# Performance work log

Measured on AMD Instinct MI355X. Metric: run time of the kernel, lower is better.

## Reference

```python
import jax, jax.numpy as jnp
import numpy as np

D = 2048          # hidden_size
N = 16            # num query heads
K = 8             # num kv heads
G = N // K        # GQA groups
H = 128           # head_dim (== head_dim_original, already padded)
T_NOISE = 1024
T_PAD = 1024
MAX_KV = 4096
THETA = 1000000.0
EPS = 1e-6
SM_SCALE = H ** -0.5
NEG = -1e30


def apply_rope(x, pos):
    # x: (T, heads, H); rotate-half (NeoX/Qwen) convention over full head_dim
    half = H // 2
    inv_freq = 1.0 / (THETA ** (jnp.arange(half, dtype=jnp.float32) / half))
    ang = pos.astype(jnp.float32)[:, None] * inv_freq[None, :]      # (T, half)
    cos = jnp.cos(ang)[:, None, :]
    sin = jnp.sin(ang)[:, None, :]
    x1, x2 = x[..., :half], x[..., half:]
    return jnp.concatenate([x1 * cos - x2 * sin, x2 * cos + x1 * sin], axis=-1)


def rms_norm(x, scale):
    var = jnp.mean(jnp.square(x), axis=-1, keepdims=True)
    return x * jax.lax.rsqrt(var + EPS) * scale


def setup_inputs() -> dict:
    key = jax.random.key(0)
    ks = jax.random.split(key, 10)
    cache_len = 1024
    actual_ctx = 768
    u = lambda k, shape: jax.random.uniform(k, shape, jnp.float32) * 0.01  # nnx uniform init
    return {
        "x_noise": jax.random.normal(ks[0], (T_NOISE, D), jnp.float32),
        "target_hidden": jax.random.normal(ks[1], (T_PAD, D), jnp.float32),
        "noise_positions": jnp.arange(T_NOISE, dtype=jnp.int32) + cache_len + actual_ctx,
        "ctx_positions": jnp.arange(T_PAD, dtype=jnp.int32) + cache_len,
        "kv_cache_k": jax.random.normal(ks[2], (1, N, MAX_KV, H), jnp.float32),
        "kv_cache_v": jax.random.normal(ks[3], (1, N, MAX_KV, H), jnp.float32),
        "cache_len": cache_len,
        "actual_ctx_count": actual_ctx,
        "Wq": u(ks[4], (D, N, H)),
        "Wk": u(ks[5], (D, K, H)),
        "Wv": u(ks[6], (D, K, H)),
        "Wo": u(ks[7], (N, H, D)),
        "q_scale": u(ks[8], (H,)),
        "k_scale": u(ks[9], (H,)),
    }


def reference(x_noise, target_hidden, noise_positions, ctx_positions,
              kv_cache_k, kv_cache_v, cache_len, actual_ctx_count,
              Wq, Wk, Wv, Wo, q_scale, k_scale):
    T_noise = x_noise.shape[0]
    T_padded = target_hidden.shape[0]
    # Q projection + RMSNorm + RoPE
    q = jnp.einsum('td,dnh->tnh', x_noise, Wq)
    q = apply_rope(rms_norm(q, q_scale), noise_positions)              # (Tq, N, H)
    # K/V over [context, noise]
    x_new = jnp.concatenate([target_hidden, x_noise], axis=0)
    k_new = jnp.einsum('td,dkh->tkh', x_new, Wk)
    v_new = jnp.einsum('td,dkh->tkh', x_new, Wv)
    new_positions = jnp.concatenate([ctx_positions, noise_positions], axis=0)
    k_new = apply_rope(rms_norm(k_new, k_scale), new_positions)
    # GQA expand before cache write (matches original)
    if G > 1:
        k_new = jnp.repeat(k_new, G, axis=1)
        v_new = jnp.repeat(v_new, G, axis=1)
    # Phase A: masked context write at cache_len
    ctx_mask = (jnp.arange(T_padded) < actual_ctx_count)[:, None, None]
    k_ctx = jnp.where(ctx_mask, k_new[:T_padded], 0.0)
    v_ctx = jnp.where(ctx_mask, v_new[:T_padded], 0.0)
    to4d = lambda a: a.transpose(1, 0, 2)[None]                        # (1, N, T, H)
    kv_cache_k = jax.lax.dynamic_update_slice(kv_cache_k, to4d(k_ctx), (0, 0, cache_len, 0))
    kv_cache_v = jax.lax.dynamic_update_slice(kv_cache_v, to4d(v_ctx), (0, 0, cache_len, 0))
    # Phase B: noise write at cache_len + actual_ctx_count
    noise_start = cache_len + actual_ctx_count
    kv_cache_k = jax.lax.dynamic_update_slice(kv_cache_k, to4d(k_new[T_padded:]), (0, 0, noise_start, 0))
    kv_cache_v = jax.lax.dynamic_update_slice(kv_cache_v, to4d(v_new[T_padded:]), (0, 0, noise_start, 0))
    new_cache_len = noise_start + T_noise
    # Non-causal attention over full cache, padding masked (segment_ids semantics)
    kv_valid = jnp.arange(MAX_KV) < new_cache_len                      # (MAX_KV,)
    scores = jnp.einsum('qnh,nkh->nqk', q, kv_cache_k[0]) * SM_SCALE   # (N, Tq, MAX_KV)
    scores = jnp.where(kv_valid[None, None, :], scores, NEG)
    probs = jax.nn.softmax(scores, axis=-1)
    attn = jnp.einsum('nqk,nkh->qnh', probs, kv_cache_v[0])            # (Tq, N, H)
    output = jnp.einsum('qnh,nhd->qd', attn, Wo)                       # (Tq, D)
    return (output, kv_cache_k, kv_cache_v)
```

## Files before the change

kernel.cpp:

```cpp
#include <hip/hip_runtime.h>
#include <hip/hip_bf16.h>
#include <math.h>

#define D 2048
#define NH 16
#define KHD 8
#define HD 128
#define T_NOISE 1024
#define T_PAD 1024
#define MAX_KV 4096
#define SM_SCALE 0.08838834764831845f

typedef __attribute__((ext_vector_type(8))) short short8;
typedef __attribute__((ext_vector_type(4))) short short4v;
typedef __attribute__((ext_vector_type(4))) float f32x4;

__device__ __forceinline__ unsigned short f2bf(float f) {
    union { float f; unsigned u; } v; v.f = f;
    unsigned r = v.u + 0x7fff + ((v.u >> 16) & 1);
    return (unsigned short)(r >> 16);
}
__device__ __forceinline__ float bf2f(short s) {
    union { unsigned u; float f; } v; v.u = ((unsigned)(unsigned short)s) << 16;
    return v.f;
}
__device__ __forceinline__ void gload16(const void* g, void* l) {
    __builtin_amdgcn_global_load_lds(
        (const __attribute__((address_space(1))) unsigned int*)g,
        (__attribute__((address_space(3))) unsigned int*)l, 16, 0, 0);
}
__device__ __forceinline__ unsigned cvtpk(float lo, float hi) {
    unsigned r;
    asm("v_cvt_pk_bf16_f32 %0, %1, %2" : "=v"(r) : "v"(lo), "v"(hi));
    return r;
}

__global__ __launch_bounds__(256)
void cast_concat(const float* __restrict__ A0, const float* __restrict__ A1,
                 short* __restrict__ out, int splitElems) {
    int i = (blockIdx.x * 256 + threadIdx.x) * 8;
    const float* src = (i < splitElems) ? (A0 + i) : (A1 + (i - splitElems));
    float4 f0 = *(const float4*)src;
    float4 f1 = *(const float4*)(src + 4);
    short8 s;
    s[0] = (short)f2bf(f0.x); s[1] = (short)f2bf(f0.y);
    s[2] = (short)f2bf(f0.z); s[3] = (short)f2bf(f0.w);
    s[4] = (short)f2bf(f1.x); s[5] = (short)f2bf(f1.y);
    s[6] = (short)f2bf(f1.z); s[7] = (short)f2bf(f1.w);
    *(short8*)(out + i) = s;
}

__global__ __launch_bounds__(256)
void conv_transpose(const float* __restrict__ W, short* __restrict__ Wt,
                    int R, int C) {
    __shared__ short t[64][72];
    int tid = threadIdx.x;
    int r0 = blockIdx.y * 64, c0 = blockIdx.x * 64;
    int rl = tid >> 4, cl4 = (tid & 15) * 4;
    #pragma unroll
    for (int j = 0; j < 4; ++j) {
        int r = rl + j * 16;
        float4 f = *(const float4*)(W + (size_t)(r0 + r) * C + c0 + cl4);
        t[cl4 + 0][r] = (short)f2bf(f.x);
        t[cl4 + 1][r] = (short)f2bf(f.y);
        t[cl4 + 2][r] = (short)f2bf(f.z);
        t[cl4 + 3][r] = (short)f2bf(f.w);
    }
    __syncthreads();
    #pragma unroll
    for (int j = 0; j < 2; ++j) {
        int idx = tid + j * 256;
        int cr = idx >> 3, rc8 = (idx & 7) * 8;
        *(short8*)(Wt + (size_t)(c0 + cr) * R + r0 + rc8) = *(const short8*)&t[cr][rc8];
    }
}

__global__ __launch_bounds__(256)
void gemm_qkv(const short* __restrict__ xbf, const short* __restrict__ Btp,
              short* __restrict__ k_tmpb, short* __restrict__ v_tmpb,
              short* __restrict__ q_tmpb) {
    const int n0 = blockIdx.x * 128;
    const int m0 = blockIdx.y * 128;
    const bool isQ = (n0 >= 2048);
    if (isQ && m0 >= 1024) return;
    const short* A = xbf + (isQ ? (size_t)1024 * 2048 : 0);

    __shared__ __align__(16) short As[128 * 32];
    __shared__ __align__(16) short Bs[128 * 32];
    const int tid = threadIdx.x;
    const int w = tid >> 6, lane = tid & 63;
    const int g = lane >> 4, li = lane & 15;
    const int wr = w >> 1, wc = w & 1;

    f32x4 acc[4][4];
    #pragma unroll
    for (int mi = 0; mi < 4; ++mi)
        #pragma unroll
        for (int ni = 0; ni < 4; ++ni) {
            acc[mi][ni][0] = 0.f; acc[mi][ni][1] = 0.f;
            acc[mi][ni][2] = 0.f; acc[mi][ni][3] = 0.f;
        }

    for (int k0 = 0; k0 < 2048; k0 += 32) {
        #pragma unroll
        for (int i = 0; i < 2; ++i) {
            int idx = i * 256 + w * 64 + lane;
            int row = idx >> 2, slot = idx & 3;
            gload16(A + (size_t)(m0 + row) * 2048 + k0 + slot * 8,
                    (char*)As + (size_t)(i * 256 + w * 64) * 16);
            gload16(Btp + (size_t)(n0 + row) * 2048 + k0 + slot * 8,
                    (char*)Bs + (size_t)(i * 256 + w * 64) * 16);
        }
        __syncthreads();
        short8 af[4], bf[4];
        #pragma unroll
        for (int mi = 0; mi < 4; ++mi)
            af[mi] = *(const short8*)&As[(wr * 64 + mi * 16 + li) * 32 + g * 8];
        #pragma unroll
        for (int ni = 0; ni < 4; ++ni)
            bf[ni] = *(const short8*)&Bs[(wc * 64 + ni * 16 + li) * 32 + g * 8];
        #pragma unroll
        for (int mi = 0; mi < 4; ++mi)
            #pragma unroll
            for (int ni = 0; ni < 4; ++ni)
                acc[mi][ni] = __builtin_amdgcn_mfma_f32_16x16x32_bf16(
                    af[mi], bf[ni], acc[mi][ni], 0, 0, 0);
        __syncthreads();
    }
    short* cp; int cbase, ldc2;
    if (n0 < 1024)      { cp = k_tmpb; cbase = 0;    ldc2 = 1024; }
    else if (n0 < 2048) { cp = v_tmpb; cbase = 1024; ldc2 = 1024; }
    else                { cp = q_tmpb; cbase = 2048; ldc2 = 2048; }
    #pragma unroll
    for (int mi = 0; mi < 4; ++mi)
        #pragma unroll
        for (int ni = 0; ni < 4; ++ni) {
            int n = n0 + wc * 64 + ni * 16 + li - cbase;
            #pragma unroll
            for (int r = 0; r < 4; ++r) {
                int m = m0 + wr * 64 + mi * 16 + 4 * g + r;
                cp[(size_t)m * ldc2 + n] = (short)f2bf(acc[mi][ni][r]);
            }
        }
}

__global__ __launch_bounds__(256)
void gemm_bf16_64(const short* __restrict__ A, const short* __restrict__ Bt,
                  float* __restrict__ C, int ldc, int K) {
    __shared__ __align__(16) short As[64 * 32];
    __shared__ __align__(16) short Bs[128 * 32];
    const int tid = threadIdx.x;
    const int w = tid >> 6, lane = tid & 63;
    const int g = lane >> 4, li = lane & 15;
    const int wr = w >> 1, wc = w & 1;
    const int m0 = blockIdx.y * 64, n0 = blockIdx.x * 128;

    f32x4 acc[2][4];
    #pragma unroll
    for (int mi = 0; mi < 2; ++mi)
        #pragma unroll
        for (int ni = 0; ni < 4; ++ni) {
            acc[mi][ni][0] = 0.f; acc[mi][ni][1] = 0.f;
            acc[mi][ni][2] = 0.f; acc[mi][ni][3] = 0.f;
        }

    for (int k0 = 0; k0 < K; k0 += 32) {
        {
            int idx = w * 64 + lane;
            int row = idx >> 2, slot = idx & 3;
            gload16(A + (size_t)(m0 + row) * K + k0 + slot * 8,
                    (char*)As + (size_t)(w * 64) * 16);
        }
        #pragma unroll
        for (int i = 0; i < 2; ++i) {
            int idx = i * 256 + w * 64 + lane;
            int row = idx >> 2, slot = idx & 3;
            gload16(Bt + (size_t)(n0 + row) * K + k0 + slot * 8,
                    (char*)Bs + (size_t)(i * 256 + w * 64) * 16);
        }
        __syncthreads();
        short8 af[2], bf[4];
        #pragma unroll
        for (int mi = 0; mi < 2; ++mi)
            af[mi] = *(const short8*)&As[(wr * 32 + mi * 16 + li) * 32 + g * 8];
        #pragma unroll
        for (int ni = 0; ni < 4; ++ni)
            bf[ni] = *(const short8*)&Bs[(wc * 64 + ni * 16 + li) * 32 + g * 8];
        #pragma unroll
        for (int mi = 0; mi < 2; ++mi)
            #pragma unroll
            for (int ni = 0; ni < 4; ++ni)
                acc[mi][ni] = __builtin_amdgcn_mfma_f32_16x16x32_bf16(
                    af[mi], bf[ni], acc[mi][ni], 0, 0, 0);
        __syncthreads();
    }
    #pragma unroll
    for (int mi = 0; mi < 2; ++mi)
        #pragma unroll
        for (int ni = 0; ni < 4; ++ni) {
            int n = n0 + wc * 64 + ni * 16 + li;
            #pragma unroll
            for (int r = 0; r < 4; ++r) {
                int m = m0 + wr * 32 + mi * 16 + 4 * g + r;
                C[(size_t)m * ldc + n] = acc[mi][ni][r];
            }
        }
}

__global__ __launch_bounds__(128)
void rmsrope_bf(short* __restrict__ x, int hpt,
                const int* __restrict__ posA, const int* __restrict__ posB,
                int splitT, const float* __restrict__ scale, float post) {
    __shared__ float red[128];
    __shared__ float nrm[128];
    int row = blockIdx.x;
    int h = threadIdx.x;
    float v = bf2f(x[(size_t)row * HD + h]);
    red[h] = v * v;
    __syncthreads();
    #pragma unroll
    for (int off = 64; off > 0; off >>= 1) {
        if (h < off) red[h] += red[h + off];
        __syncthreads();
    }
    float inv = rsqrtf(red[0] * (1.0f / 128.0f) + 1e-6f);
    nrm[h] = v * inv * scale[h];
    __syncthreads();
    if (h < 64) {
        int t = row / hpt;
        int pos = (t < splitT) ? posA[t] : posB[t - splitT];
        float inv_freq = expf((float)h * (-13.815510557964274f / 64.0f));
        float ang = (float)pos * inv_freq;
        float c = cosf(ang), s = sinf(ang);
        float x1 = nrm[h], x2 = nrm[h + 64];
        x[(size_t)row * HD + h]      = (short)f2bf((x1 * c - x2 * s) * post);
        x[(size_t)row * HD + h + 64] = (short)f2bf((x2 * c + x1 * s) * post);
    }
}

__global__ __launch_bounds__(256)
void cache_scatter2(const float* __restrict__ in_k, const float* __restrict__ in_v,
                    const short* __restrict__ k_tmpb, const short* __restrict__ v_tmpb,
                    float* __restrict__ out_k, float* __restrict__ out_v,
                    short* __restrict__ kbf, short* __restrict__ vbf,
                    const int* __restrict__ clp, const int* __restrict__ acp) {
    const int cache_len = clp[0], actx = acp[0];
    const int noise_start = cache_len + actx;
    const int new_len = noise_start + T_NOISE;
    int i = blockIdx.x * 256 + threadIdx.x;
    int n = i >> 16;
    int rem = i & 65535;
    int pos = rem >> 4;
    int h8 = (rem & 15) << 3;
    size_t co = ((size_t)(n * MAX_KV + pos)) * HD + h8;
    short8 ks8, vs8;
    if (pos >= cache_len && pos < new_len) {
        int tkn = (pos < noise_start) ? (pos - cache_len) : (T_PAD + (pos - noise_start));
        size_t so = ((size_t)(tkn * KHD + (n >> 1))) * HD + h8;
        ks8 = *(const short8*)(k_tmpb + so);
        vs8 = *(const short8*)(v_tmpb + so);
        float4 a, b;
        a.x = bf2f(ks8[0]); a.y = bf2f(ks8[1]); a.z = bf2f(ks8[2]); a.w = bf2f(ks8[3]);
        b.x = bf2f(ks8[4]); b.y = bf2f(ks8[5]); b.z = bf2f(ks8[6]); b.w = bf2f(ks8[7]);
        *(float4*)(out_k + co) = a; *(float4*)(out_k + co + 4) = b;
        a.x = bf2f(vs8[0]); a.y = bf2f(vs8[1]); a.z = bf2f(vs8[2]); a.w = bf2f(vs8[3]);
        b.x = bf2f(vs8[4]); b.y = bf2f(vs8[5]); b.z = bf2f(vs8[6]); b.w = bf2f(vs8[7]);
        *(float4*)(out_v + co) = a; *(float4*)(out_v + co + 4) = b;
    } else {
        float4 ka = *(const float4*)(in_k + co);
        float4 kb = *(const float4*)(in_k + co + 4);
        float4 va = *(const float4*)(in_v + co);
        float4 vb = *(const float4*)(in_v + co + 4);
        *(float4*)(out_k + co) = ka; *(float4*)(out_k + co + 4) = kb;
        *(float4*)(out_v + co) = va; *(float4*)(out_v + co + 4) = vb;
        ks8[0] = (short)f2bf(ka.x); ks8[1] = (short)f2bf(ka.y);
        ks8[2] = (short)f2bf(ka.z); ks8[3] = (short)f2bf(ka.w);
        ks8[4] = (short)f2bf(kb.x); ks8[5] = (short)f2bf(kb.y);
        ks8[6] = (short)f2bf(kb.z); ks8[7] = (short)f2bf(kb.w);
        vs8[0] = (short)f2bf(va.x); vs8[1] = (short)f2bf(va.y);
        vs8[2] = (short)f2bf(va.z); vs8[3] = (short)f2bf(va.w);
        vs8[4] = (short)f2bf(vb.x); vs8[5] = (short)f2bf(vb.y);
        vs8[6] = (short)f2bf(vb.z); vs8[7] = (short)f2bf(vb.w);
    }
    *(short8*)(kbf + co) = ks8;
    *(short8*)(vbf + co) = vs8;
}

#define VBUF(b) ((b) * 16896)

__device__ __forceinline__ short4v tr_read(unsigned addr) {
    short4v d;
    asm volatile("ds_read_b64_tr_b16 %0, %1" : "=v"(d) : "v"(addr));
    return d;
}

__global__ __launch_bounds__(128, 2)
void attn_mfma(const short* __restrict__ qbf, const short* __restrict__ kbf,
               const short* __restrict__ vbf, short* __restrict__ opA,
               short* __restrict__ opB, float* __restrict__ mlpart,
               const int* __restrict__ clp, const int* __restrict__ acp) {
    __shared__ __align__(16) char smem[33792];
    const int tid  = threadIdx.x;
    const int w    = tid >> 6;
    const int lane = tid & 63;
    const int g    = lane >> 4;
    const int li   = lane & 15;
    const int bid  = blockIdx.x;
    const int head = 2 * (bid & 7) + ((bid >> 3) & 1);
    const int rest = bid >> 4;
    const int q0   = (rest & 15) * 64;
    const int kvs  = rest >> 4;
    const int new_len = clp[0] + acp[0] + T_NOISE;
    const int ntiles  = (new_len + 63) >> 6;
    const int ntq     = (ntiles + 3) >> 2;

    const short* kb_g = kbf + (size_t)head * MAX_KV * HD;
    const short* vb_g = vbf + (size_t)head * MAX_KV * HD;

    short8 qf[2][4];
    #pragma unroll
    for (int sub = 0; sub < 2; ++sub) {
        const short* qp = qbf + ((size_t)(q0 + w * 32 + sub * 16 + li) * NH + head) * HD;
        #pragma unroll
        for (int ks = 0; ks < 4; ++ks) qf[sub][ks] = *(const short8*)(qp + 32 * ks + 8 * g);
    }

    f32x4 acc[2][8];
    #pragma unroll
    for (int sub = 0; sub < 2; ++sub)
        #pragma unroll
        for (int n = 0; n < 8; ++n) {
            acc[sub][n][0] = 0.f; acc[sub][n][1] = 0.f;
            acc[sub][n][2] = 0.f; acc[sub][n][3] = 0.f;
        }
    float m[2], l[2];
    m[0] = -INFINITY; m[1] = -INFINITY; l[0] = 0.f; l[1] = 0.f;

    const int vrloc = 4 * (lane >> 3) + ((lane >> 1) & 3);
    const int vcof  = (lane & 1) * 8;

    auto STAGE = [&](int tt, int bb) {
        const int base = (kvs * ntq + tt) * 64;
        #pragma unroll
        for (int half = 0; half < 2; ++half)
            #pragma unroll
            for (int i2 = 0; i2 < 4; ++i2) {
                const int ht = w * 4 + i2;
                gload16(vb_g + ((size_t)(base + half * 32 + vrloc) << 7) + ht * 16 + vcof,
                        smem + VBUF(bb) + half * 8448 + ht * 1056);
            }
    };

    short8 kpre[16];
    auto KLOAD = [&](int tt) {
        const int kp0 = (kvs * ntq + tt) << 6;
        const short* kr = kb_g + ((size_t)(kp0 + li) << 7) + g * 8;
        #pragma unroll
        for (int ks = 0; ks < 4; ++ks)
            #pragma unroll
            for (int j = 0; j < 4; ++j)
                kpre[ks * 4 + j] = *(const short8*)(kr + (size_t)(j * 16) * HD + ks * 32);
    };

    auto mkfrag = [&](const float* pA, const float* pB) -> short8 {
        unsigned w0 = cvtpk(pA[0], pA[1]), w1 = cvtpk(pA[2], pA[3]);
        unsigned w2 = cvtpk(pB[0], pB[1]), w3 = cvtpk(pB[2], pB[3]);
        const bool lowg = (g < 2);
        unsigned a0 = lowg ? w2 : w0, a1 = lowg ? w3 : w1;
        unsigned r0 = __shfl_xor((int)a0, 32), r1 = __shfl_xor((int)a1, 32);
        unsigned o0 = lowg ? w0 : w2, o1 = lowg ? w1 : w3;
        const bool sendOwn = (g == 1 || g == 2);
        unsigned b0 = sendOwn ? o0 : r0, b1 = sendOwn ? o1 : r1;
        unsigned g0_ = __shfl_xor((int)b0, 16), g1_ = __shfl_xor((int)b1, 16);
        union { unsigned u[4]; short8 s; } pau;
        pau.u[0] = (g == 0) ? o0 : (g == 2) ? r0 : g0_;
        pau.u[1] = (g == 0) ? o1 : (g == 2) ? r1 : g1_;
        pau.u[2] = (g == 3) ? o0 : (g == 1) ? r0 : g0_;
        pau.u[3] = (g == 3) ? o1 : (g == 1) ? r1 : g1_;
        return pau.s;
    };

    KLOAD(0);
    STAGE(0, 0);
    __syncthreads();

    for (int t = 0; t < ntq; ++t) {
        const int b = t & 1;
        if (t + 1 < ntq) STAGE(t + 1, b ^ 1);
        const int pos0 = (kvs * ntq + t) << 6;
        f32x4 s[4][2];
        #pragma unroll
        for (int j = 0; j < 4; ++j)
            #pragma unroll
            for (int sub = 0; sub < 2; ++sub) {
                s[j][sub][0] = 0.f; s[j][sub][1] = 0.f;
                s[j][sub][2] = 0.f; s[j][sub][3] = 0.f;
            }
        #pragma unroll
        for (int ks = 0; ks < 4; ++ks)
            #pragma unroll
            for (int j = 0; j < 4; ++j) {
                short8 kf = kpre[ks * 4 + j];
                s[j][0] = __builtin_amdgcn_mfma_f32_16x16x32_bf16(kf, qf[0][ks], s[j][0], 0, 0, 0);
                s[j][1] = __builtin_amdgcn_mfma_f32_16x16x32_bf16(kf, qf[1][ks], s[j][1], 0, 0, 0);
            }
        if (t + 1 < ntq) KLOAD(t + 1);
        #pragma unroll
        for (int j = 0; j < 4; ++j)
            #pragma unroll
            for (int r = 0; r < 4; ++r)
                if (pos0 + 16 * j + 4 * g + r >= new_len) {
                    s[j][0][r] = -1e30f; s[j][1][r] = -1e30f;
                }
        short8 pa[2][2];
        #pragma unroll
        for (int sub = 0; sub < 2; ++sub) {
            float tm = -INFINITY;
            #pragma unroll
            for (int j = 0; j < 4; ++j)
                #pragma unroll
                for (int r = 0; r < 4; ++r) tm = fmaxf(tm, s[j][sub][r]);
            tm = fmaxf(tm, __shfl_xor(tm, 16));
            tm = fmaxf(tm, __shfl_xor(tm, 32));
            if (tm > m[sub] + 8.f) {
                const float alpha = __expf(m[sub] - tm);
                m[sub] = tm;
                l[sub] *= alpha;
                #pragma unroll
                for (int n = 0; n < 8; ++n) {
                    acc[sub][n][0] *= alpha; acc[sub][n][1] *= alpha;
                    acc[sub][n][2] *= alpha; acc[sub][n][3] *= alpha;
                }
            }
            const float mb = m[sub];
            float p[4][4];
            float rs = 0.f;
            #pragma unroll
            for (int j = 0; j < 4; ++j)
                #pragma unroll
                for (int r = 0; r < 4; ++r) {
                    p[j][r] = __expf(s[j][sub][r] - mb);
                    rs += p[j][r];
                }
            rs += __shfl_xor(rs, 16);
            rs += __shfl_xor(rs, 32);
            l[sub] += rs;
            pa[sub][0] = mkfrag(p[0], p[1]);
            pa[sub][1] = mkfrag(p[2], p[3]);
        }
        #pragma unroll
        for (int half = 0; half < 2; ++half) {
            const unsigned vb0 = (unsigned)(size_t)(smem + VBUF(b)) + half * 8448
                               + g * 256 + li * 8;
            short4v vt[16];
            #pragma unroll
            for (int h2 = 0; h2 < 8; ++h2) {
                vt[2 * h2]     = tr_read(vb0 + h2 * 1056);
                vt[2 * h2 + 1] = tr_read(vb0 + h2 * 1056 + 128);
            }
            asm volatile("s_waitcnt lgkmcnt(0)" ::: "memory");
            __builtin_amdgcn_sched_barrier(0);
            #pragma unroll
            for (int h2 = 0; h2 < 8; ++h2) {
                short8 vf = __builtin_shufflevector(vt[2 * h2], vt[2 * h2 + 1],
                                                    0, 1, 2, 3, 4, 5, 6, 7);
                acc[0][h2] = __builtin_amdgcn_mfma_f32_16x16x32_bf16(vf, pa[0][half], acc[0][h2], 0, 0, 0);
                acc[1][h2] = __builtin_amdgcn_mfma_f32_16x16x32_bf16(vf, pa[1][half], acc[1][h2], 0, 0, 0);
            }
        }
        __syncthreads();
    }

    short* op = (kvs < 2) ? (opA + (size_t)kvs * 16 * 1024 * 128)
                          : (opB + (size_t)(kvs - 2) * 16 * 1024 * 128);
    #pragma unroll
    for (int sub = 0; sub < 2; ++sub) {
        const int qrow = q0 + w * 32 + sub * 16 + li;
        const size_t ro = ((size_t)(head << 10) + qrow) * 128;
        #pragma unroll
        for (int n = 0; n < 8; ++n) {
            short4v o4;
            o4[0] = (short)f2bf(acc[sub][n][0]); o4[1] = (short)f2bf(acc[sub][n][1]);
            o4[2] = (short)f2bf(acc[sub][n][2]); o4[3] = (short)f2bf(acc[sub][n][3]);
            *(short4v*)(op + ro + 16 * n + 4 * g) = o4;
        }
        if (g == 0) {
            float* ml = mlpart + (((size_t)(kvs * 16 + head) << 10) + qrow) * 2;
            ml[0] = m[sub]; ml[1] = l[sub];
        }
    }
}

__global__ __launch_bounds__(256)
void attn_merge(const short* __restrict__ opA, const short* __restrict__ opB,
                const float* __restrict__ mlpart, short* __restrict__ a_bf) {
    int gid = blockIdx.x * 256 + threadIdx.x;
    int row = gid >> 4;
    int c8  = (gid & 15) * 8;
    int head = row >> 10, q = row & 1023;
    float mg[4], lg[4], mstar = -INFINITY;
    #pragma unroll
    for (int s = 0; s < 4; ++s) {
        const float* ml = mlpart + (((size_t)(s * 16 + head) << 10) + q) * 2;
        mg[s] = ml[0]; lg[s] = ml[1];
        mstar = fmaxf(mstar, mg[s]);
    }
    float cg[4], lstar = 0.f;
    #pragma unroll
    for (int s = 0; s < 4; ++s) { cg[s] = __expf(mg[s] - mstar); lstar += lg[s] * cg[s]; }
    const float inv = 1.0f / lstar;
    float o[8] = {};
    #pragma unroll
    for (int s = 0; s < 4; ++s) {
        const short* op = (s < 2) ? (opA + (size_t)s * 16 * 1024 * 128)
                                  : (opB + (size_t)(s - 2) * 16 * 1024 * 128);
        short8 v = *(const short8*)(op + (((size_t)(head << 10)) + q) * 128 + c8);
        #pragma unroll
        for (int j = 0; j < 8; ++j) o[j] += cg[s] * bf2f(v[j]);
    }
    short8 o8;
    #pragma unroll
    for (int j = 0; j < 8; ++j) o8[j] = (short)f2bf(o[j] * inv);
    *(short8*)(a_bf + (size_t)q * 2048 + head * 128 + c8) = o8;
}

extern "C" void kernel_launch(void* const* d_in, const int* in_sizes, int n_in,
                              void* d_out, int out_size, void* d_ws, size_t ws_size,
                              hipStream_t stream) {
    const float* x_noise       = (const float*)d_in[0];
    const float* target_hidden = (const float*)d_in[1];
    const int*   noise_pos     = (const int*)d_in[2];
    const int*   ctx_pos       = (const int*)d_in[3];
    const float* in_k          = (const float*)d_in[4];
    const float* in_v          = (const float*)d_in[5];
    const int*   clp           = (const int*)d_in[6];
    const int*   acp           = (const int*)d_in[7];
    const float* Wq            = (const float*)d_in[8];
    const float* Wk            = (const float*)d_in[9];
    const float* Wv            = (const float*)d_in[10];
    const float* Wo            = (const float*)d_in[11];
    const float* q_scale       = (const float*)d_in[12];
    const float* k_scale       = (const float*)d_in[13];

    float* out   = (float*)d_out;
    float* out_k = out + (size_t)T_NOISE * D;
    float* out_v = out_k + (size_t)NH * MAX_KV * HD;

    float* ws     = (float*)d_ws;
    const size_t M1 = 1024u * 1024u;
    short* q_tmpb = (short*)ws;
    short* a_bf   = q_tmpb;
    short* k_tmpb = (short*)(ws + 1 * M1);
    short* v_tmpb = (short*)(ws + 2 * M1);
    float* mlpart = (float*)v_tmpb;
    short* xbf    = (short*)(ws + 3 * M1);
    short* opartA = xbf;
    short* btpack = (short*)(ws + 5 * M1);
    short* wo_t   = btpack;
    short* opartB = (short*)(ws + 7 * M1);
    short* kbf    = (short*)(ws + 9 * M1);
    short* vbf    = (short*)(ws + 13 * M1);

    dim3 blk(256);
    cast_concat<<<2048, blk, 0, stream>>>(target_hidden, x_noise, xbf, 1024 * 2048);
    conv_transpose<<<dim3(16, 32), blk, 0, stream>>>(Wk, btpack, 2048, 1024);
    conv_transpose<<<dim3(16, 32), blk, 0, stream>>>(Wv, btpack + (size_t)1024 * 2048, 2048, 1024);
    conv_transpose<<<dim3(32, 32), blk, 0, stream>>>(Wq, btpack + (size_t)2048 * 2048, 2048, 2048);
    gemm_qkv<<<dim3(32, 16), blk, 0, stream>>>(xbf, btpack, k_tmpb, v_tmpb, q_tmpb);
    conv_transpose<<<dim3(32, 32), blk, 0, stream>>>(Wo, wo_t, 2048, 2048);
    rmsrope_bf<<<1024 * 16, 128, 0, stream>>>(q_tmpb, NH, noise_pos, noise_pos, 2048,
                                              q_scale, SM_SCALE);
    rmsrope_bf<<<2048 * 8, 128, 0, stream>>>(k_tmpb, KHD, ctx_pos, noise_pos, 1024,
                                             k_scale, 1.0f);
    cache_scatter2<<<4096, blk, 0, stream>>>(in_k, in_v, k_tmpb, v_tmpb,
                                             out_k, out_v, kbf, vbf, clp, acp);
    attn_mfma<<<1024, 128, 0, stream>>>(q_tmpb, kbf, vbf, opartA, opartB, mlpart, clp, acp);
    attn_merge<<<1024, blk, 0, stream>>>(opartA, opartB, mlpart, a_bf);
    gemm_bf16_64<<<dim3(16, 16), blk, 0, stream>>>(a_bf, wo_t, out, 2048, 2048);
}
```

Measured before the change: 223.9 us.

## Software-pipeline QK MFMA of next tile under V LDS transpose reads

Moves the QK^T score computation for tile t+1 into iteration t, issuing it while the transposed V reads from LDS are in flight, and prefetches K for t+2. The goal is to hide LDS read latency behind MFMA work and raise matrix-core utilisation. It also adds s_setprio around the MFMA blocks and skips the padding mask unless the tile crosses new_len. In exchange the score accumulators stay live across iterations, which raises register pressure and could lower occupancy.

```diff
diff --git a/kernel.cpp b/kernel.cpp
--- a/kernel.cpp
+++ b/kernel.cpp
@@ -362,6 +362,25 @@
                 kpre[ks * 4 + j] = *(const short8*)(kr + (size_t)(j * 16) * HD + ks * 32);
     };
 
+    f32x4 s[4][2];
+    auto QK = [&]() {
+        #pragma unroll
+        for (int j = 0; j < 4; ++j)
+            #pragma unroll
+            for (int sub = 0; sub < 2; ++sub) {
+                s[j][sub][0] = 0.f; s[j][sub][1] = 0.f;
+                s[j][sub][2] = 0.f; s[j][sub][3] = 0.f;
+            }
+        #pragma unroll
+        for (int ks = 0; ks < 4; ++ks)
+            #pragma unroll
+            for (int j = 0; j < 4; ++j) {
+                short8 kf = kpre[ks * 4 + j];
+                s[j][0] = __builtin_amdgcn_mfma_f32_16x16x32_bf16(kf, qf[0][ks], s[j][0], 0, 0, 0);
+                s[j][1] = __builtin_amdgcn_mfma_f32_16x16x32_bf16(kf, qf[1][ks], s[j][1], 0, 0, 0);
+            }
+    };
+
     auto mkfrag = [&](const float* pA, const float* pB) -> short8 {
         unsigned w0 = cvtpk(pA[0], pA[1]), w1 = cvtpk(pA[2], pA[3]);
         unsigned w2 = cvtpk(pB[0], pB[1]), w3 = cvtpk(pB[2], pB[3]);
@@ -383,35 +402,22 @@
     KLOAD(0);
     STAGE(0, 0);
     __syncthreads();
+    QK();
+    if (ntq > 1) KLOAD(1);
 
     for (int t = 0; t < ntq; ++t) {
         const int b = t & 1;
         if (t + 1 < ntq) STAGE(t + 1, b ^ 1);
         const int pos0 = (kvs * ntq + t) << 6;
-        f32x4 s[4][2];
-        #pragma unroll
-        for (int j = 0; j < 4; ++j)
-            #pragma unroll
-            for (int sub = 0; sub < 2; ++sub) {
-                s[j][sub][0] = 0.f; s[j][sub][1] = 0.f;
-                s[j][sub][2] = 0.f; s[j][sub][3] = 0.f;
-            }
-        #pragma unroll
-        for (int ks = 0; ks < 4; ++ks)
-            #pragma unroll
-            for (int j = 0; j < 4; ++j) {
-                short8 kf = kpre[ks * 4 + j];
-                s[j][0] = __builtin_amdgcn_mfma_f32_16x16x32_bf16(kf, qf[0][ks], s[j][0], 0, 0, 0);
-                s[j][1] = __builtin_amdgcn_mfma_f32_16x16x32_bf16(kf, qf[1][ks], s[j][1], 0, 0, 0);
-            }
-        if (t + 1 < ntq) KLOAD(t + 1);
-        #pragma unroll
-        for (int j = 0; j < 4; ++j)
-            #pragma unroll
-            for (int r = 0; r < 4; ++r)
-                if (pos0 + 16 * j + 4 * g + r >= new_len) {
-                    s[j][0][r] = -1e30f; s[j][1][r] = -1e30f;
-                }
+        if (pos0 + 63 >= new_len) {
+            #pragma unroll
+            for (int j = 0; j < 4; ++j)
+                #pragma unroll
+                for (int r = 0; r < 4; ++r)
+                    if (pos0 + 16 * j + 4 * g + r >= new_len) {
+                        s[j][0][r] = -1e30f; s[j][1][r] = -1e30f;
+                    }
+        }
         short8 pa[2][2];
         #pragma unroll
         for (int sub = 0; sub < 2; ++sub) {
@@ -448,25 +454,48 @@
             pa[sub][0] = mkfrag(p[0], p[1]);
             pa[sub][1] = mkfrag(p[2], p[3]);
         }
-        #pragma unroll
-        for (int half = 0; half < 2; ++half) {
-            const unsigned vb0 = (unsigned)(size_t)(smem + VBUF(b)) + half * 8448
-                               + g * 256 + li * 8;
+        {
+            const unsigned vb0 = (unsigned)(size_t)(smem + VBUF(b)) + g * 256 + li * 8;
             short4v vt[16];
             #pragma unroll
             for (int h2 = 0; h2 < 8; ++h2) {
                 vt[2 * h2]     = tr_read(vb0 + h2 * 1056);
                 vt[2 * h2 + 1] = tr_read(vb0 + h2 * 1056 + 128);
             }
+            if (t + 1 < ntq) {
+                __builtin_amdgcn_s_setprio(1);
+                QK();
+                __builtin_amdgcn_s_setprio(0);
+                if (t + 2 < ntq) KLOAD(t + 2);
+            }
             asm volatile("s_waitcnt lgkmcnt(0)" ::: "memory");
             __builtin_amdgcn_sched_barrier(0);
+            __builtin_amdgcn_s_setprio(1);
             #pragma unroll
             for (int h2 = 0; h2 < 8; ++h2) {
                 short8 vf = __builtin_shufflevector(vt[2 * h2], vt[2 * h2 + 1],
                                                     0, 1, 2, 3, 4, 5, 6, 7);
-                acc[0][h2] = __builtin_amdgcn_mfma_f32_16x16x32_bf16(vf, pa[0][half], acc[0][h2], 0, 0, 0);
-                acc[1][h2] = __builtin_amdgcn_mfma_f32_16x16x32_bf16(vf, pa[1][half], acc[1][h2], 0, 0, 0);
-            }
+                acc[0][h2] = __builtin_amdgcn_mfma_f32_16x16x32_bf16(vf, pa[0][0], acc[0][h2], 0, 0, 0);
+                acc[1][h2] = __builtin_amdgcn_mfma_f32_16x16x32_bf16(vf, pa[1][0], acc[1][h2], 0, 0, 0);
+            }
+            __builtin_amdgcn_s_setprio(0);
+            const unsigned vb1 = vb0 + 8448;
+            #pragma unroll
+            for (int h2 = 0; h2 < 8; ++h2) {
+                vt[2 * h2]     = tr_read(vb1 + h2 * 1056);
+                vt[2 * h2 + 1] = tr_read(vb1 + h2 * 1056 + 128);
+            }
+            asm volatile("s_waitcnt lgkmcnt(0)" ::: "memory");
+            __builtin_amdgcn_sched_barrier(0);
+            __builtin_amdgcn_s_setprio(1);
+            #pragma unroll
+            for (int h2 = 0; h2 < 8; ++h2) {
+                short8 vf = __builtin_shufflevector(vt[2 * h2], vt[2 * h2 + 1],
+                                                    0, 1, 2, 3, 4, 5, 6, 7);
+                acc[0][h2] = __builtin_amdgcn_mfma_f32_16x16x32_bf16(vf, pa[0][1], acc[0][h2], 0, 0, 0);
+                acc[1][h2] = __builtin_amdgcn_mfma_f32_16x16x32_bf16(vf, pa[1][1], acc[1][h2], 0, 0, 0);
+            }
+            __builtin_amdgcn_s_setprio(0);
         }
         __syncthreads();
     }
```

Result: slower. 248.1 us (+10.8%).
